# Kernel tuning notes

Hardware: AMD Instinct MI355X
Metric: run time of the kernel (lower is better)

## Reference

```python
import jax, jax.numpy as jnp
import numpy as np

N = 20000      # nodes
E = 320000     # edges
IN = 300       # input_channel
HID = 100      # hidden_channel (= heads*out_channels with heads=1)
R = 50         # num_relations
B = 8          # num_bases (the 4th positional arg 'heads'=8 lands on num_bases in PyG RGATConv)
HEADS = 1
CLS = 3
Q = 64         # number of query (aspect) nodes
EPS = 1e-16


def setup_inputs() -> dict:
    key = jax.random.key(0)
    ks = jax.random.split(key, 16)
    x = jax.random.normal(ks[0], (N, IN), jnp.float32)
    edge_index = jax.random.randint(ks[1], (2, E), 0, N)
    edge_type = jax.random.randint(ks[2], (E,), 0, R)
    query_indices = jax.random.randint(ks[3], (Q,), 0, N)

    def w(k, shape, scale):
        return jax.random.normal(k, shape, jnp.float32) * scale

    comp1 = w(ks[4], (R, B), 0.3)
    basis1 = w(ks[5], (B, IN, HEADS * HID), 1.0 / np.sqrt(IN))
    q1 = w(ks[6], (HEADS * HID, HEADS), 0.1)
    k1 = w(ks[7], (HEADS * HID, HEADS), 0.1)
    b1 = jnp.zeros((HEADS * HID,), jnp.float32)
    comp2 = w(ks[8], (R, B), 0.3)
    basis2 = w(ks[9], (B, HID, HEADS * HID), 1.0 / np.sqrt(HID))
    q2 = w(ks[10], (HEADS * HID, HEADS), 0.1)
    k2 = w(ks[11], (HEADS * HID, HEADS), 0.1)
    b2 = jnp.zeros((HEADS * HID,), jnp.float32)
    Wl = w(ks[12], (CLS, HID), 1.0 / np.sqrt(HID))
    bl = jnp.zeros((CLS,), jnp.float32)
    return dict(x=x, edge_index=edge_index, edge_type=edge_type,
                query_indices=query_indices,
                comp1=comp1, basis1=basis1, q1=q1, k1=k1, b1=b1,
                comp2=comp2, basis2=basis2, q2=q2, k2=k2, b2=b2,
                Wl=Wl, bl=bl)


def segment_softmax(alpha, seg, num_segments):
    # numerically-stable softmax over edges grouped by destination node
    m = jax.ops.segment_max(alpha, seg, num_segments=num_segments)  # [N, H]
    e = jnp.exp(alpha - m[seg])
    s = jax.ops.segment_sum(e, seg, num_segments=num_segments)
    return e / (s[seg] + EPS)


def rgat_conv(x, edge_index, edge_type, comp, basis, q, k, b):
    # basis-decomposed per-relation weight: [R, in, H*out]
    W = jnp.einsum('rb,bio->rio', comp, basis)
    # transform every node under every relation once, then gather per edge
    xt = jnp.einsum('ni,rio->nro', x, W)          # [N, R, H*out]
    src, dst = edge_index[0], edge_index[1]        # j -> i (source_to_target)
    xi = xt[dst, edge_type]                        # [E, H*out]
    xj = xt[src, edge_type]                        # [E, H*out]
    qi = xi @ q                                    # [E, H]
    kj = xj @ k                                    # [E, H]
    alpha = jax.nn.leaky_relu(qi + kj, 0.2)        # additive self-attention
    alpha = segment_softmax(alpha, dst, N)         # across-relation softmax
    msg = xj.reshape(E, HEADS, HID) * alpha[:, :, None]
    out = jax.ops.segment_sum(msg, dst, num_segments=N)  # [N, H, out]
    return out.reshape(N, HEADS * HID) + b         # concat=True


def reference(x, edge_index, edge_type, query_indices,
              comp1, basis1, q1, k1, b1,
              comp2, basis2, q2, k2, b2, Wl, bl):
    h = jax.nn.relu(rgat_conv(x, edge_index, edge_type, comp1, basis1, q1, k1, b1))
    h = jax.nn.relu(rgat_conv(h, edge_index, edge_type, comp2, basis2, q2, k2, b2))
    pooled = h[query_indices].mean(axis=0)          # [HID]
    return pooled @ Wl.T + bl                       # [CLS]
```

## Files before the change

### kernel.cpp

```cpp
#include <hip/hip_runtime.h>
#include <math.h>

#define N_NODES 20000
#define E_EDGES 320000
#define IN_CH   300
#define HID     100
#define R_REL   50
#define NB      8
#define CLS     3
#define NQ      64
#define OUTW    800
#define ZW      128
#define SCAN_BLKS ((N_NODES + 255) / 256)

typedef unsigned short ushort_t;
typedef __attribute__((ext_vector_type(8))) short     short8;
typedef __attribute__((ext_vector_type(8))) unsigned short ushort8;
typedef __attribute__((ext_vector_type(4))) float     f32x4;
typedef __attribute__((ext_vector_type(2))) float     f32x2;

__device__ __forceinline__ ushort_t f2bf_rne(float f) {
    unsigned u = __float_as_uint(f);
    unsigned r = (u + 0x7fffu + ((u >> 16) & 1u)) >> 16;
    return (ushort_t)r;
}
__device__ __forceinline__ float bf2f(ushort_t u) {
    return __uint_as_float((unsigned)u << 16);
}

__global__ __launch_bounds__(256) void zero_deg2(int* __restrict__ dd,
                                                 int* __restrict__ ds) {
    int i = blockIdx.x * 256 + threadIdx.x;
    if (i < N_NODES) { dd[i] = 0; ds[i] = 0; }
}

__global__ __launch_bounds__(256) void hist2_kernel(
        const int* __restrict__ ei, int* __restrict__ dd,
        int* __restrict__ ds) {
    int e = blockIdx.x * 256 + threadIdx.x;
    if (e < E_EDGES) {
        atomicAdd(&dd[ei[E_EDGES + e]], 1);
        atomicAdd(&ds[ei[e]], 1);
    }
}

__global__ __launch_bounds__(256) void scan1_both(
        const int* __restrict__ deg_d, int* __restrict__ rp_d, int* __restrict__ bsum_d,
        const int* __restrict__ deg_s, int* __restrict__ rp_s, int* __restrict__ bsum_s) {
    int set = blockIdx.x / SCAN_BLKS, blk = blockIdx.x % SCAN_BLKS;
    const int* deg = set ? deg_s : deg_d;
    int* rowptr    = set ? rp_s  : rp_d;
    int* bsum      = set ? bsum_s : bsum_d;
    __shared__ int s[256];
    int tid = threadIdx.x;
    int idx = blk * 256 + tid;
    int v = (idx < N_NODES) ? deg[idx] : 0;
    s[tid] = v; __syncthreads();
    #pragma unroll
    for (int off = 1; off < 256; off <<= 1) {
        int t = (tid >= off) ? s[tid - off] : 0;
        __syncthreads();
        s[tid] += t;
        __syncthreads();
    }
    if (idx < N_NODES) rowptr[idx] = s[tid] - v;
    if (tid == 255) bsum[blk] = s[255];
}

__global__ __launch_bounds__(128) void scan2_both(
        int* __restrict__ bsum_d, int* __restrict__ rp_d,
        int* __restrict__ bsum_s, int* __restrict__ rp_s) {
    int* bsum   = blockIdx.x ? bsum_s : bsum_d;
    int* rowptr = blockIdx.x ? rp_s   : rp_d;
    __shared__ int s[128];
    int tid = threadIdx.x;
    int v = (tid < SCAN_BLKS) ? bsum[tid] : 0;
    s[tid] = v; __syncthreads();
    #pragma unroll
    for (int off = 1; off < 128; off <<= 1) {
        int t = (tid >= off) ? s[tid - off] : 0;
        __syncthreads();
        s[tid] += t;
        __syncthreads();
    }
    if (tid < SCAN_BLKS) bsum[tid] = s[tid] - v;
    if (tid == 0) rowptr[N_NODES] = E_EDGES;
}

__global__ __launch_bounds__(256) void scan3_both(
        int* __restrict__ rp_d, const int* __restrict__ bsum_d, int* __restrict__ cur_d,
        int* __restrict__ rp_s, const int* __restrict__ bsum_s, int* __restrict__ cur_s) {
    int set = blockIdx.x / SCAN_BLKS, blk = blockIdx.x % SCAN_BLKS;
    int* rowptr      = set ? rp_s   : rp_d;
    const int* bsum  = set ? bsum_s : bsum_d;
    int* cursor      = set ? cur_s  : cur_d;
    int idx = blk * 256 + threadIdx.x;
    if (idx < N_NODES) {
        int v = rowptr[idx] + bsum[blk];
        rowptr[idx] = v;
        cursor[idx] = v;
    }
}

__global__ __launch_bounds__(256) void scatter_both(
        const int* __restrict__ ei, const int* __restrict__ et,
        int* __restrict__ cur_d, int* __restrict__ cur_s,
        int* __restrict__ skey, int* __restrict__ skey_s) {
    int e = blockIdx.x * 256 + threadIdx.x;
    if (e >= E_EDGES) return;
    int s = ei[e], d = ei[E_EDGES + e], rt = et[e];
    int p = atomicAdd(&cur_d[d], 1);
    skey[p] = (s << 6) | rt;
    int qp = atomicAdd(&cur_s[s], 1);
    skey_s[qp] = (p << 6) | rt;
}

__global__ __launch_bounds__(256) void split_bt_kernel(
        const float* __restrict__ basis, ushort_t* __restrict__ Bt,
        int K, int Kp) {
    int idx = blockIdx.x * 256 + threadIdx.x;
    if (idx >= OUTW * Kp) return;
    int n = idx / Kp, k = idx - n * Kp;
    int b = n / HID, o = n - b * HID;
    float v = 0.f;
    if (k < K) v = basis[((size_t)b * K + k) * HID + o];
    Bt[idx] = f2bf_rne(v);
}

#define BM 32
#define BN 160
#define NCB (OUTW / BN)
__global__ __launch_bounds__(256) void gemm_mfma(
        const float* __restrict__ A, const ushort_t* __restrict__ Bt,
        ushort_t* __restrict__ xbh, int M, int K, int Kp, int do_relu) {
    __shared__ ushort_t As[BM * 328];
    __shared__ ushort_t Bs[BN * 32];
    int tid  = threadIdx.x;
    int lane = tid & 63, wave = tid >> 6;
    int ml = lane & 15, quad = lane >> 4;
    int wr = (wave >> 1) * 16, wc = (wave & 1) * 80;
    int row0 = blockIdx.x * BM;
    int SW = Kp + 8;
    int ksteps = Kp >> 5;

    {
        int ra = tid >> 3;
        int gr = row0 + ra;
        const float* ar = A + (size_t)gr * K;
        for (int c = (tid & 7); c * 8 < Kp; c += 8) {
            int kb = c * 8;
            float vals[8];
            if (gr < M) {
                if (kb + 8 <= K) {
                    float4 f0 = *(const float4*)&ar[kb];
                    float4 f1 = *(const float4*)&ar[kb + 4];
                    vals[0]=f0.x; vals[1]=f0.y; vals[2]=f0.z; vals[3]=f0.w;
                    vals[4]=f1.x; vals[5]=f1.y; vals[6]=f1.z; vals[7]=f1.w;
                } else {
                    #pragma unroll
                    for (int i = 0; i < 8; i++)
                        vals[i] = (kb + i < K) ? ar[kb + i] : 0.f;
                }
                if (do_relu)
                    #pragma unroll
                    for (int i = 0; i < 8; i++) vals[i] = fmaxf(vals[i], 0.f);
            } else {
                #pragma unroll
                for (int i = 0; i < 8; i++) vals[i] = 0.f;
            }
            ushort8 hv;
            #pragma unroll
            for (int i = 0; i < 8; i++) hv[i] = f2bf_rne(vals[i]);
            *(ushort8*)&As[ra * SW + kb] = hv;
        }
    }

    for (int cb = 0; cb < NCB; cb++) {
        int col0 = cb * BN;
        f32x4 acc[5] = {};
        for (int ks = 0; ks < ksteps; ks++) {
            int k0 = ks << 5;
            __syncthreads();
            for (int t = tid; t < 640; t += 256) {
                int rb = t >> 2, ch = t & 3;
                __builtin_amdgcn_global_load_lds(
                    (const __attribute__((address_space(1))) unsigned int*)
                        &Bt[(size_t)(col0 + rb) * Kp + k0 + ch * 8],
                    (__attribute__((address_space(3))) unsigned int*)&Bs[t * 8],
                    16, 0, 0);
            }
            __syncthreads();
            short8 af, bf[5];
            af = *(const short8*)&As[(wr + ml) * SW + k0 + quad * 8];
            #pragma unroll
            for (int nt = 0; nt < 5; nt++)
                bf[nt] = *(const short8*)&Bs[(wc + nt * 16 + ml) * 32 + quad * 8];
            #pragma unroll
            for (int nt = 0; nt < 5; nt++)
                acc[nt] = __builtin_amdgcn_mfma_f32_16x16x32_bf16(af, bf[nt], acc[nt], 0, 0, 0);
        }
        #pragma unroll
        for (int nt = 0; nt < 5; nt++) {
            #pragma unroll
            for (int r = 0; r < 4; r++) {
                int grow = row0 + wr + quad * 4 + r;
                if (grow < M)
                    xbh[(size_t)grow * OUTW + col0 + wc + nt * 16 + ml] =
                        f2bf_rne(acc[nt][r]);
            }
        }
    }
}

__global__ __launch_bounds__(256) void qbkb_kernel(
        const float* __restrict__ basis, const float* __restrict__ q,
        const float* __restrict__ k, float* __restrict__ qb,
        float* __restrict__ kb, int K) {
    int idx = blockIdx.x * 256 + threadIdx.x;
    if (idx >= K * NB) return;
    int kk = idx >> 3, b = idx & 7;
    const float* br = basis + ((size_t)b * K + kk) * HID;
    float aq = 0.f, ak = 0.f;
    for (int o = 0; o < HID; o++) {
        float v = br[o];
        aq = fmaf(v, q[o], aq);
        ak = fmaf(v, k[o], ak);
    }
    qb[idx] = aq; kb[idx] = ak;
}

__global__ __launch_bounds__(256) void qk2_kernel(
        const float* __restrict__ x, const float* __restrict__ qb,
        const float* __restrict__ kb, float* __restrict__ xbq,
        float* __restrict__ xbk, int K, int do_relu) {
    __shared__ float sqb[320 * NB], skb[320 * NB];
    int tid = threadIdx.x;
    for (int i = tid; i < K * NB; i += 256) { sqb[i] = qb[i]; skb[i] = kb[i]; }
    __syncthreads();
    int idx = blockIdx.x * 256 + tid;
    if (idx >= N_NODES * NB) return;
    int n = idx >> 3, b = idx & 7;
    const float* xr = x + (size_t)n * K;
    float aq = 0.f, ak = 0.f;
    for (int kk = 0; kk < K; kk++) {
        float v = xr[kk];
        if (do_relu) v = fmaxf(v, 0.f);
        aq = fmaf(v, sqb[kk * NB + b], aq);
        ak = fmaf(v, skb[kk * NB + b], ak);
    }
    xbq[idx] = aq;
    xbk[idx] = ak;
}

__global__ __launch_bounds__(256) void compute_z(
        const int* __restrict__ rowptr_s, const int* __restrict__ skey_s,
        const float* __restrict__ comp, const ushort_t* __restrict__ xbh,
        ushort_t* __restrict__ Z) {
    int wave = threadIdx.x >> 6, lane = threadIdx.x & 63;
    int s = blockIdx.x * 4 + wave;
    if (s >= N_NODES) return;
    int beg = rowptr_s[s], end = rowptr_s[s + 1];
    if (beg == end) return;
    int o = lane * 2;
    f32x2 xrow[NB];
    if (lane < 50) {
        #pragma unroll
        for (int b = 0; b < NB; b++) {
            ushort2 xx = *(const ushort2*)&xbh[(size_t)s * OUTW + b * HID + o];
            xrow[b].x = bf2f(xx.x);
            xrow[b].y = bf2f(xx.y);
        }
    }
    for (int p = beg; p < end; p++) {
        int key = skey_s[p];
        int zpos = key >> 6, rt = key & 63;
        const float* cr = comp + rt * NB;
        if (lane < 50) {
            f32x2 z = {0.f, 0.f};
            #pragma unroll
            for (int b = 0; b < NB; b++) z += cr[b] * xrow[b];
            ushort2 zz;
            zz.x = f2bf_rne(z.x);
            zz.y = f2bf_rne(z.y);
            *(ushort2*)&Z[(size_t)zpos * ZW + o] = zz;
        }
    }
}

__global__ __launch_bounds__(256) void msg_soft(
        const int* __restrict__ rowptr, const int* __restrict__ skey,
        const float* __restrict__ comp, const ushort_t* __restrict__ Z,
        const float* __restrict__ xbq, const float* __restrict__ xbk,
        const float* __restrict__ bias, float* __restrict__ h) {
    int wave = threadIdx.x >> 6, lane = threadIdx.x & 63;
    int d = blockIdx.x * 4 + wave;
    if (d >= N_NODES) return;
    int beg = rowptr[d], end = rowptr[d + 1];

    float4 qd0 = *(const float4*)&xbq[d * NB];
    float4 qd1 = *(const float4*)&xbq[d * NB + 4];

    f32x2 acc = {0.f, 0.f};
    float m = -1e30f, l = 0.f;
    int o = lane * 2;

    for (int c0 = beg; c0 < end; c0 += 64) {
        int p = c0 + lane;
        bool valid = p < end;
        float a = -1e30f;
        if (valid) {
            int key = skey[p];
            int s = key >> 6, rt = key & 63;
            const float4 c0v = *(const float4*)&comp[rt * NB];
            const float4 c1v = *(const float4*)&comp[rt * NB + 4];
            const float4 k0v = *(const float4*)&xbk[s * NB];
            const float4 k1v = *(const float4*)&xbk[s * NB + 4];
            float qi = c0v.x*qd0.x + c0v.y*qd0.y + c0v.z*qd0.z + c0v.w*qd0.w
                     + c1v.x*qd1.x + c1v.y*qd1.y + c1v.z*qd1.z + c1v.w*qd1.w;
            float kj = c0v.x*k0v.x + c0v.y*k0v.y + c0v.z*k0v.z + c0v.w*k0v.w
                     + c1v.x*k1v.x + c1v.y*k1v.y + c1v.z*k1v.z + c1v.w*k1v.w;
            a = qi + kj;
            a = a > 0.f ? a : 0.2f * a;
        }
        float cm = a;
        #pragma unroll
        for (int off = 32; off; off >>= 1) cm = fmaxf(cm, __shfl_xor(cm, off));
        float M = fmaxf(m, cm);
        float scale = __expf(m - M);
        acc *= scale; l *= scale; m = M;
        float wgt = valid ? __expf(a - M) : 0.f;
        float cs = wgt;
        #pragma unroll
        for (int off = 32; off; off >>= 1) cs += __shfl_xor(cs, off);
        l += cs;
        int cnt = end - c0; if (cnt > 64) cnt = 64;
        for (int j = 0; j < cnt; j++) {
            float wj = __shfl(wgt, j);
            if (lane < 50) {
                ushort2 zz = *(const ushort2*)&Z[(size_t)(c0 + j) * ZW + o];
                f32x2 zv = {bf2f(zz.x), bf2f(zz.y)};
                acc += wj * zv;
            }
        }
    }
    if (lane < 50) {
        float inv = 1.f / (l + 1e-16f);
        f32x2 r;
        r.x = bias[o]     + acc.x * inv;
        r.y = bias[o + 1] + acc.y * inv;
        *(f32x2*)&h[(size_t)d * HID + o] = r;
    }
}

__global__ __launch_bounds__(128) void head_kernel(
        const float* __restrict__ h2, const int* __restrict__ qidx,
        const float* __restrict__ Wl, const float* __restrict__ bl,
        float* __restrict__ out) {
    __shared__ float pooled[HID];
    int tid = threadIdx.x;
    if (tid < HID) {
        float s = 0.f;
        for (int i = 0; i < NQ; i++)
            s += fmaxf(h2[(size_t)qidx[i] * HID + tid], 0.f);
        pooled[tid] = s * (1.0f / NQ);
    }
    __syncthreads();
    if (tid < CLS) {
        float s = bl[tid];
        for (int o = 0; o < HID; o++) s = fmaf(pooled[o], Wl[tid * HID + o], s);
        out[tid] = s;
    }
}

extern "C" void kernel_launch(void* const* d_in, const int* in_sizes, int n_in,
                              void* d_out, int out_size, void* d_ws, size_t ws_size,
                              hipStream_t stream) {
    const float* x      = (const float*)d_in[0];
    const int*   ei     = (const int*)  d_in[1];
    const int*   et     = (const int*)  d_in[2];
    const int*   qidx   = (const int*)  d_in[3];
    const float* comp1  = (const float*)d_in[4];
    const float* basis1 = (const float*)d_in[5];
    const float* q1     = (const float*)d_in[6];
    const float* k1     = (const float*)d_in[7];
    const float* b1     = (const float*)d_in[8];
    const float* comp2  = (const float*)d_in[9];
    const float* basis2 = (const float*)d_in[10];
    const float* q2     = (const float*)d_in[11];
    const float* k2     = (const float*)d_in[12];
    const float* b2     = (const float*)d_in[13];
    const float* Wl     = (const float*)d_in[14];
    const float* bl     = (const float*)d_in[15];
    float* out = (float*)d_out;

    const int KP1 = 320, KP2 = 128;

    char* w = (char*)d_ws;
    size_t off = 0;
    auto alloc = [&](size_t nbytes) {
        void* p = (void*)(w + off);
        off += ((nbytes + 255) / 256) * 256;
        return p;
    };
    ushort_t* xbh    = (ushort_t*)alloc((size_t)N_NODES * OUTW * 2);
    ushort_t* Z      = (ushort_t*)alloc((size_t)E_EDGES * ZW * 2);
    float*    h1     = (float*)alloc((size_t)N_NODES * HID * 4);
    float*    h2     = (float*)alloc((size_t)N_NODES * HID * 4);
    ushort_t* Bt     = (ushort_t*)alloc((size_t)OUTW * KP1 * 2);
    float*    xbq    = (float*)alloc((size_t)N_NODES * NB * 4);
    float*    xbk    = (float*)alloc((size_t)N_NODES * NB * 4);
    float*    qb     = (float*)alloc((size_t)KP1 * NB * 4);
    float*    kb     = (float*)alloc((size_t)KP1 * NB * 4);
    int*      deg_d  = (int*)alloc(N_NODES * 4);
    int*      deg_s  = (int*)alloc(N_NODES * 4);
    int*      rp_d   = (int*)alloc((N_NODES + 1) * 4);
    int*      rp_s   = (int*)alloc((N_NODES + 1) * 4);
    int*      cur_d  = (int*)alloc(N_NODES * 4);
    int*      cur_s  = (int*)alloc(N_NODES * 4);
    int*      bsum_d = (int*)alloc(SCAN_BLKS * 4);
    int*      bsum_s = (int*)alloc(SCAN_BLKS * 4);
    int*      skey   = (int*)alloc(E_EDGES * 4);
    int*      skey_s = (int*)alloc(E_EDGES * 4);

    zero_deg2<<<SCAN_BLKS, 256, 0, stream>>>(deg_d, deg_s);
    hist2_kernel<<<(E_EDGES + 255) / 256, 256, 0, stream>>>(ei, deg_d, deg_s);
    scan1_both<<<2 * SCAN_BLKS, 256, 0, stream>>>(deg_d, rp_d, bsum_d, deg_s, rp_s, bsum_s);
    scan2_both<<<2, 128, 0, stream>>>(bsum_d, rp_d, bsum_s, rp_s);
    scan3_both<<<2 * SCAN_BLKS, 256, 0, stream>>>(rp_d, bsum_d, cur_d, rp_s, bsum_s, cur_s);
    scatter_both<<<(E_EDGES + 255) / 256, 256, 0, stream>>>(ei, et, cur_d, cur_s, skey, skey_s);

    auto layer = [&](const float* input, int K, int Kp, int relu_in,
                     const float* comp, const float* basis, const float* q,
                     const float* k, const float* bias, float* hout) {
        int nb = OUTW * Kp;
        split_bt_kernel<<<(nb + 255) / 256, 256, 0, stream>>>(basis, Bt, K, Kp);
        gemm_mfma<<<(N_NODES + BM - 1) / BM, 256, 0, stream>>>(input, Bt, xbh, N_NODES, K, Kp, relu_in);
        qbkb_kernel<<<(K * NB + 255) / 256, 256, 0, stream>>>(basis, q, k, qb, kb, K);
        qk2_kernel<<<(N_NODES * NB + 255) / 256, 256, 0, stream>>>(input, qb, kb, xbq, xbk, K, relu_in);
        compute_z<<<(N_NODES + 3) / 4, 256, 0, stream>>>(rp_s, skey_s, comp, xbh, Z);
        msg_soft<<<(N_NODES + 3) / 4, 256, 0, stream>>>(rp_d, skey, comp, Z, xbq, xbk, bias, hout);
    };

    layer(x,  IN_CH, KP1, 0, comp1, basis1, q1, k1, b1, h1);
    layer(h1, HID,   KP2, 1, comp2, basis2, q2, k2, b2, h2);
    head_kernel<<<1, 128, 0, stream>>>(h2, qidx, Wl, bl, out);
}
```

Before: 412.8 us.

## Write Z in source order with gather index, split GEMM columns across grid, fuse prep kernels

compute_z now writes each edge's Z row contiguously in source-sorted order, and msg_soft gathers rows through a new zidx permutation. This makes the writes sequential, and Z rows shrink from 128 to 100 bf16 elements, so the buffer is smaller. The GEMM puts column blocks on a second grid dimension instead of looping over them, which gives more blocks but restages the A tile once per column block. The basis split and q/k basis projections are fused into one launch, trading a gathered read in msg_soft for cheaper writes and fewer launches.

```diff
diff --git a/kernel.cpp b/kernel.cpp
--- a/kernel.cpp
+++ b/kernel.cpp
@@ -10,7 +10,7 @@
 #define CLS     3
 #define NQ      64
 #define OUTW    800
-#define ZW      128
+#define ZW      100
 #define SCAN_BLKS ((N_NODES + 255) / 256)
 
 typedef unsigned short ushort_t;
@@ -105,31 +105,49 @@
 __global__ __launch_bounds__(256) void scatter_both(
         const int* __restrict__ ei, const int* __restrict__ et,
         int* __restrict__ cur_d, int* __restrict__ cur_s,
-        int* __restrict__ skey, int* __restrict__ skey_s) {
+        int* __restrict__ skey, int* __restrict__ skey_s,
+        int* __restrict__ zidx) {
     int e = blockIdx.x * 256 + threadIdx.x;
     if (e >= E_EDGES) return;
     int s = ei[e], d = ei[E_EDGES + e], rt = et[e];
     int p = atomicAdd(&cur_d[d], 1);
     skey[p] = (s << 6) | rt;
     int qp = atomicAdd(&cur_s[s], 1);
-    skey_s[qp] = (p << 6) | rt;
-}
-
-__global__ __launch_bounds__(256) void split_bt_kernel(
-        const float* __restrict__ basis, ushort_t* __restrict__ Bt,
-        int K, int Kp) {
-    int idx = blockIdx.x * 256 + threadIdx.x;
-    if (idx >= OUTW * Kp) return;
-    int n = idx / Kp, k = idx - n * Kp;
-    int b = n / HID, o = n - b * HID;
-    float v = 0.f;
-    if (k < K) v = basis[((size_t)b * K + k) * HID + o];
-    Bt[idx] = f2bf_rne(v);
+    skey_s[qp] = rt;
+    zidx[p] = qp;
+}
+
+__global__ __launch_bounds__(256) void prep_kernel(
+        const float* __restrict__ basis, const float* __restrict__ q,
+        const float* __restrict__ k, ushort_t* __restrict__ Bt,
+        float* __restrict__ qb, float* __restrict__ kb,
+        int K, int Kp, int split_blocks) {
+    int bx = blockIdx.x;
+    if (bx < split_blocks) {
+        int idx = bx * 256 + threadIdx.x;
+        if (idx >= OUTW * Kp) return;
+        int n = idx / Kp, kk = idx - n * Kp;
+        int b = n / HID, o = n - b * HID;
+        float v = 0.f;
+        if (kk < K) v = basis[((size_t)b * K + kk) * HID + o];
+        Bt[idx] = f2bf_rne(v);
+    } else {
+        int idx = (bx - split_blocks) * 256 + threadIdx.x;
+        if (idx >= K * NB) return;
+        int kk = idx >> 3, b = idx & 7;
+        const float* br = basis + ((size_t)b * K + kk) * HID;
+        float aq = 0.f, ak = 0.f;
+        for (int o = 0; o < HID; o++) {
+            float v = br[o];
+            aq = fmaf(v, q[o], aq);
+            ak = fmaf(v, k[o], ak);
+        }
+        qb[idx] = aq; kb[idx] = ak;
+    }
 }
 
 #define BM 32
 #define BN 160
-#define NCB (OUTW / BN)
 __global__ __launch_bounds__(256) void gemm_mfma(
         const float* __restrict__ A, const ushort_t* __restrict__ Bt,
         ushort_t* __restrict__ xbh, int M, int K, int Kp, int do_relu) {
@@ -140,6 +158,7 @@
     int ml = lane & 15, quad = lane >> 4;
     int wr = (wave >> 1) * 16, wc = (wave & 1) * 80;
     int row0 = blockIdx.x * BM;
+    int col0 = blockIdx.y * BN;
     int SW = Kp + 8;
     int ksteps = Kp >> 5;
 
@@ -175,58 +194,38 @@
         }
     }
 
-    for (int cb = 0; cb < NCB; cb++) {
-        int col0 = cb * BN;
-        f32x4 acc[5] = {};
-        for (int ks = 0; ks < ksteps; ks++) {
-            int k0 = ks << 5;
-            __syncthreads();
-            for (int t = tid; t < 640; t += 256) {
-                int rb = t >> 2, ch = t & 3;
-                __builtin_amdgcn_global_load_lds(
-                    (const __attribute__((address_space(1))) unsigned int*)
-                        &Bt[(size_t)(col0 + rb) * Kp + k0 + ch * 8],
-                    (__attribute__((address_space(3))) unsigned int*)&Bs[t * 8],
-                    16, 0, 0);
-            }
-            __syncthreads();
-            short8 af, bf[5];
-            af = *(const short8*)&As[(wr + ml) * SW + k0 + quad * 8];
-            #pragma unroll
-            for (int nt = 0; nt < 5; nt++)
-                bf[nt] = *(const short8*)&Bs[(wc + nt * 16 + ml) * 32 + quad * 8];
-            #pragma unroll
-            for (int nt = 0; nt < 5; nt++)
-                acc[nt] = __builtin_amdgcn_mfma_f32_16x16x32_bf16(af, bf[nt], acc[nt], 0, 0, 0);
-        }
-        #pragma unroll
-        for (int nt = 0; nt < 5; nt++) {
-            #pragma unroll
-            for (int r = 0; r < 4; r++) {
-                int grow = row0 + wr + quad * 4 + r;
-                if (grow < M)
-                    xbh[(size_t)grow * OUTW + col0 + wc + nt * 16 + ml] =
-                        f2bf_rne(acc[nt][r]);
-            }
-        }
-    }
-}
-
-__global__ __launch_bounds__(256) void qbkb_kernel(
-        const float* __restrict__ basis, const float* __restrict__ q,
-        const float* __restrict__ k, float* __restrict__ qb,
-        float* __restrict__ kb, int K) {
-    int idx = blockIdx.x * 256 + threadIdx.x;
-    if (idx >= K * NB) return;
-    int kk = idx >> 3, b = idx & 7;
-    const float* br = basis + ((size_t)b * K + kk) * HID;
-    float aq = 0.f, ak = 0.f;
-    for (int o = 0; o < HID; o++) {
-        float v = br[o];
-        aq = fmaf(v, q[o], aq);
-        ak = fmaf(v, k[o], ak);
-    }
-    qb[idx] = aq; kb[idx] = ak;
+    f32x4 acc[5] = {};
+    for (int ks = 0; ks < ksteps; ks++) {
+        int k0 = ks << 5;
+        __syncthreads();
+        for (int t = tid; t < 640; t += 256) {
+            int rb = t >> 2, ch = t & 3;
+            __builtin_amdgcn_global_load_lds(
+                (const __attribute__((address_space(1))) unsigned int*)
+                    &Bt[(size_t)(col0 + rb) * Kp + k0 + ch * 8],
+                (__attribute__((address_space(3))) unsigned int*)&Bs[t * 8],
+                16, 0, 0);
+        }
+        __syncthreads();
+        short8 af, bf[5];
+        af = *(const short8*)&As[(wr + ml) * SW + k0 + quad * 8];
+        #pragma unroll
+        for (int nt = 0; nt < 5; nt++)
+            bf[nt] = *(const short8*)&Bs[(wc + nt * 16 + ml) * 32 + quad * 8];
+        #pragma unroll
+        for (int nt = 0; nt < 5; nt++)
+            acc[nt] = __builtin_amdgcn_mfma_f32_16x16x32_bf16(af, bf[nt], acc[nt], 0, 0, 0);
+    }
+    #pragma unroll
+    for (int nt = 0; nt < 5; nt++) {
+        #pragma unroll
+        for (int r = 0; r < 4; r++) {
+            int grow = row0 + wr + quad * 4 + r;
+            if (grow < M)
+                xbh[(size_t)grow * OUTW + col0 + wc + nt * 16 + ml] =
+                    f2bf_rne(acc[nt][r]);
+        }
+    }
 }
 
 __global__ __launch_bounds__(256) void qk2_kernel(
@@ -272,8 +271,7 @@
         }
     }
     for (int p = beg; p < end; p++) {
-        int key = skey_s[p];
-        int zpos = key >> 6, rt = key & 63;
+        int rt = skey_s[p] & 63;
         const float* cr = comp + rt * NB;
         if (lane < 50) {
             f32x2 z = {0.f, 0.f};
@@ -282,13 +280,14 @@
             ushort2 zz;
             zz.x = f2bf_rne(z.x);
             zz.y = f2bf_rne(z.y);
-            *(ushort2*)&Z[(size_t)zpos * ZW + o] = zz;
+            *(ushort2*)&Z[(size_t)p * ZW + o] = zz;
         }
     }
 }
 
 __global__ __launch_bounds__(256) void msg_soft(
         const int* __restrict__ rowptr, const int* __restrict__ skey,
+        const int* __restrict__ zidx,
         const float* __restrict__ comp, const ushort_t* __restrict__ Z,
         const float* __restrict__ xbq, const float* __restrict__ xbk,
         const float* __restrict__ bias, float* __restrict__ h) {
@@ -308,8 +307,10 @@
         int p = c0 + lane;
         bool valid = p < end;
         float a = -1e30f;
+        int zi = 0;
         if (valid) {
             int key = skey[p];
+            zi = zidx[p];
             int s = key >> 6, rt = key & 63;
             const float4 c0v = *(const float4*)&comp[rt * NB];
             const float4 c1v = *(const float4*)&comp[rt * NB + 4];
@@ -336,8 +337,9 @@
         int cnt = end - c0; if (cnt > 64) cnt = 64;
         for (int j = 0; j < cnt; j++) {
             float wj = __shfl(wgt, j);
+            int   zj = __shfl(zi, j);
             if (lane < 50) {
-                ushort2 zz = *(const ushort2*)&Z[(size_t)(c0 + j) * ZW + o];
+                ushort2 zz = *(const ushort2*)&Z[(size_t)zj * ZW + o];
                 f32x2 zv = {bf2f(zz.x), bf2f(zz.y)};
                 acc += wj * zv;
             }
@@ -421,24 +423,27 @@
     int*      bsum_s = (int*)alloc(SCAN_BLKS * 4);
     int*      skey   = (int*)alloc(E_EDGES * 4);
     int*      skey_s = (int*)alloc(E_EDGES * 4);
+    int*      zidx   = (int*)alloc(E_EDGES * 4);
 
     zero_deg2<<<SCAN_BLKS, 256, 0, stream>>>(deg_d, deg_s);
     hist2_kernel<<<(E_EDGES + 255) / 256, 256, 0, stream>>>(ei, deg_d, deg_s);
     scan1_both<<<2 * SCAN_BLKS, 256, 0, stream>>>(deg_d, rp_d, bsum_d, deg_s, rp_s, bsum_s);
     scan2_both<<<2, 128, 0, stream>>>(bsum_d, rp_d, bsum_s, rp_s);
     scan3_both<<<2 * SCAN_BLKS, 256, 0, stream>>>(rp_d, bsum_d, cur_d, rp_s, bsum_s, cur_s);
-    scatter_both<<<(E_EDGES + 255) / 256, 256, 0, stream>>>(ei, et, cur_d, cur_s, skey, skey_s);
+    scatter_both<<<(E_EDGES + 255) / 256, 256, 0, stream>>>(ei, et, cur_d, cur_s, skey, skey_s, zidx);
 
     auto layer = [&](const float* input, int K, int Kp, int relu_in,
                      const float* comp, const float* basis, const float* q,
                      const float* k, const float* bias, float* hout) {
-        int nb = OUTW * Kp;
-        split_bt_kernel<<<(nb + 255) / 256, 256, 0, stream>>>(basis, Bt, K, Kp);
-        gemm_mfma<<<(N_NODES + BM - 1) / BM, 256, 0, stream>>>(input, Bt, xbh, N_NODES, K, Kp, relu_in);
-        qbkb_kernel<<<(K * NB + 255) / 256, 256, 0, stream>>>(basis, q, k, qb, kb, K);
+        int split_blocks = (OUTW * Kp + 255) / 256;
+        int qb_blocks = (K * NB + 255) / 256;
+        prep_kernel<<<split_blocks + qb_blocks, 256, 0, stream>>>(
+            basis, q, k, Bt, qb, kb, K, Kp, split_blocks);
+        dim3 g((N_NODES + BM - 1) / BM, OUTW / BN);
+        gemm_mfma<<<g, 256, 0, stream>>>(input, Bt, xbh, N_NODES, K, Kp, relu_in);
         qk2_kernel<<<(N_NODES * NB + 255) / 256, 256, 0, stream>>>(input, qb, kb, xbq, xbk, K, relu_in);
         compute_z<<<(N_NODES + 3) / 4, 256, 0, stream>>>(rp_s, skey_s, comp, xbh, Z);
-        msg_soft<<<(N_NODES + 3) / 4, 256, 0, stream>>>(rp_d, skey, comp, Z, xbq, xbk, bias, hout);
+        msg_soft<<<(N_NODES + 3) / 4, 256, 0, stream>>>(rp_d, skey, zidx, comp, Z, xbq, xbk, bias, hout);
     };
 
     layer(x,  IN_CH, KP1, 0, comp1, basis1, q1, k1, b1, h1);
```

Measured after the change: 412.7 us. No clear change (-0.0%).
